# Kernel optimization log

Measured on AMD Instinct MI355X. Metric: run time of the kernel, lower is better.

## Reference

```python
import jax, jax.numpy as jnp
import numpy as np

D_MODEL = 1024
N_HEADS = 16
D_K = D_MODEL // N_HEADS
NEG = -1e10


def setup_inputs() -> dict:
    key = jax.random.key(0)
    ks = jax.random.split(key, 12)
    bs, sl = 2, 2048
    q = jax.random.normal(ks[0], (bs, sl, D_MODEL), dtype=jnp.float32)
    k = jax.random.normal(ks[1], (bs, sl, D_MODEL), dtype=jnp.float32)
    v = jax.random.normal(ks[2], (bs, sl, D_MODEL), dtype=jnp.float32)
    mask = jax.random.randint(ks[3], (bs, 1, sl, sl), 0, 2).astype(bool)
    s = 1.0 / np.sqrt(D_MODEL)
    Wq = jax.random.uniform(ks[4], (D_MODEL, D_MODEL), jnp.float32, -s, s)
    bq = jax.random.uniform(ks[5], (D_MODEL,), jnp.float32, -s, s)
    Wk = jax.random.uniform(ks[6], (D_MODEL, D_MODEL), jnp.float32, -s, s)
    bk = jax.random.uniform(ks[7], (D_MODEL,), jnp.float32, -s, s)
    Wv = jax.random.uniform(ks[8], (D_MODEL, D_MODEL), jnp.float32, -s, s)
    bv = jax.random.uniform(ks[9], (D_MODEL,), jnp.float32, -s, s)
    Wo = jax.random.uniform(ks[10], (D_MODEL, D_MODEL), jnp.float32, -s, s)
    bo = jax.random.uniform(ks[11], (D_MODEL,), jnp.float32, -s, s)
    return {"q": q, "k": k, "v": v, "mask": mask,
            "Wq": Wq, "bq": bq, "Wk": Wk, "bk": bk,
            "Wv": Wv, "bv": bv, "Wo": Wo, "bo": bo}


def reference(q, k, v, mask, Wq, bq, Wk, bk, Wv, bv, Wo, bo):
    bs, sl, _ = q.shape
    sl2 = k.shape[1]
    # linear projections (torch Linear: x @ W.T + b), split into heads: [b, h, s, d_k]
    qh = (q @ Wq.T + bq).reshape(bs, sl, N_HEADS, D_K).transpose(0, 2, 1, 3)
    kh = (k @ Wk.T + bk).reshape(bs, sl2, N_HEADS, D_K).transpose(0, 2, 1, 3)
    vh = (v @ Wv.T + bv).reshape(bs, sl2, N_HEADS, D_K).transpose(0, 2, 1, 3)
    scores = jnp.einsum('bhqd,bhkd->bhqk', qh, kh) / jnp.sqrt(jnp.float32(D_K))
    scores = jnp.where(mask, NEG, scores)
    attn = jax.nn.softmax(scores, axis=-1)
    z = jnp.einsum('bhqk,bhkd->bhqd', attn, vh)  # [b, h, sl, d_k]
    z = z.transpose(0, 2, 1, 3).reshape(bs, sl, D_MODEL)
    return z @ Wo.T + bo
```

## Files before the change

kernel.cpp:

```cpp
#include <hip/hip_runtime.h>

typedef __attribute__((ext_vector_type(8))) short short8;
typedef __attribute__((ext_vector_type(4))) float f32x4;
typedef __attribute__((ext_vector_type(16))) float f32x16;
typedef __attribute__((ext_vector_type(4))) unsigned int u32x4;

#define MFMA16(a, b, c) __builtin_amdgcn_mfma_f32_16x16x32_bf16((a), (b), (c), 0, 0, 0)
#define MFMA32(a, b, c) __builtin_amdgcn_mfma_f32_32x32x16_bf16((a), (b), (c), 0, 0, 0)

#if __has_builtin(__builtin_amdgcn_exp2f)
#define EXP2(x) __builtin_amdgcn_exp2f(x)
#else
#define EXP2(x) __expf((x) * 0.6931471805599453f)
#endif

__device__ __forceinline__ unsigned short f2bf(float f) {
  unsigned int u = __float_as_uint(f);
  u += 0x7FFFu + ((u >> 16) & 1u);
  return (unsigned short)(u >> 16);
}

__device__ __forceinline__ float bf2f(unsigned short u) {
  return __uint_as_float(((unsigned int)u) << 16);
}

__device__ __forceinline__ unsigned int cvtpk(float lo, float hi) {
  unsigned int r;
  asm("v_cvt_pk_bf16_f32 %0, %1, %2" : "=v"(r) : "v"(lo), "v"(hi));
  return r;
}

__device__ __forceinline__ short8 mk8(unsigned int a, unsigned int b,
                                      unsigned int c, unsigned int d) {
  u32x4 u = {a, b, c, d};
  return __builtin_bit_cast(short8, u);
}

__device__ __forceinline__ void gload16(const void* g, void* l) {
  __builtin_amdgcn_global_load_lds((const __attribute__((address_space(1))) void*)g,
                                   (__attribute__((address_space(3))) void*)l, 16, 0, 0);
}

__device__ __forceinline__ short8 fragld64(const unsigned short* base, int row, int kchunk) {
  int cc = kchunk ^ (row & 7);
  return *(const short8*)(base + row * 64 + cc * 8);
}

__global__ void cvt3(const float* __restrict__ a, const float* __restrict__ b,
                     const float* __restrict__ c, unsigned short* __restrict__ out, int n4) {
  const float* src = (blockIdx.z == 0) ? a : ((blockIdx.z == 1) ? b : c);
  int i = blockIdx.x * blockDim.x + threadIdx.x;
  if (i >= n4) return;
  float4 v = ((const float4*)src)[i];
  ushort4 o;
  o.x = f2bf(v.x); o.y = f2bf(v.y); o.z = f2bf(v.z); o.w = f2bf(v.w);
  ((ushort4*)(out + (size_t)blockIdx.z * (size_t)n4 * 4))[i] = o;
}

__global__ void cvt4(const float* __restrict__ a, const float* __restrict__ b,
                     const float* __restrict__ c, const float* __restrict__ d,
                     unsigned short* __restrict__ out, int n4) {
  const float* src = (blockIdx.z == 0) ? a : ((blockIdx.z == 1) ? b
                   : ((blockIdx.z == 2) ? c : d));
  int i = blockIdx.x * blockDim.x + threadIdx.x;
  if (i >= n4) return;
  float4 v = ((const float4*)src)[i];
  ushort4 o;
  o.x = f2bf(v.x); o.y = f2bf(v.y); o.z = f2bf(v.z); o.w = f2bf(v.w);
  ((ushort4*)(out + (size_t)blockIdx.z * (size_t)n4 * 4))[i] = o;
}

__global__ void maskpack(const int* __restrict__ m, unsigned long long* __restrict__ mw) {
  const int lane = threadIdx.x & 63;
  const size_t wbase = ((size_t)blockIdx.x * (blockDim.x >> 6) + (threadIdx.x >> 6)) * 4ull;
#pragma unroll
  for (int u = 0; u < 4; ++u) {
    size_t word = wbase + u;
    int x = m[word * 64 + lane];
    unsigned long long bb = __ballot(x != 0);
    if (lane == 0) mw[word] = bb;
  }
}

__global__ void vtrans(const unsigned short* __restrict__ vh, unsigned short* __restrict__ vtg) {
  __shared__ unsigned short t[64][66];
  const int sx = blockIdx.x * 64, h = blockIdx.y, b = blockIdx.z;
  const int tid = threadIdx.x;
  const int r = tid >> 2, c0 = (tid & 3) * 16;
  const unsigned short* src = vh + ((size_t)(b * 2048 + sx + r)) * 1024 + h * 64 + c0;
  short8 x0 = *(const short8*)src;
  short8 x1 = *(const short8*)(src + 8);
#pragma unroll
  for (int e = 0; e < 8; ++e) {
    t[c0 + e][r] = (unsigned short)x0[e];
    t[c0 + 8 + e][r] = (unsigned short)x1[e];
  }
  __syncthreads();
  short8 y0, y1;
#pragma unroll
  for (int e = 0; e < 8; ++e) {
    y0[e] = (short)t[r][c0 + e];
    y1[e] = (short)t[r][c0 + 8 + e];
  }
  unsigned short* dst = vtg + ((size_t)((b * 16 + h) * 64 + r)) * 2048 + sx + c0;
  *(short8*)dst = y0;
  *(short8*)(dst + 8) = y1;
}

template<bool OUT_BF16>
__global__ __launch_bounds__(256, 3) void gemm_bt(
    const unsigned short* __restrict__ Abase, const unsigned short* __restrict__ Bbase,
    const float* __restrict__ bias0, const float* __restrict__ bias1,
    const float* __restrict__ bias2, void* __restrict__ outv, float scale0)
{
  constexpr int K = 1024, N = 1024;
  const int z = blockIdx.z;
  const unsigned short* A = Abase + (size_t)z * 4194304ull;
  const unsigned short* B = Bbase + (size_t)z * 1048576ull;
  const float* bias = (z == 0) ? bias0 : ((z == 1) ? bias1 : bias2);
  const float scale = (z == 0) ? scale0 : 1.0f;

  __shared__ unsigned short ldsA[128 * 64];
  __shared__ unsigned short ldsB[128 * 64];

  const int tid = threadIdx.x;
  const int lane = tid & 63, wid = tid >> 6;
  const int c16 = lane & 15, g = lane >> 4;
  const int m0 = blockIdx.y * 128, n0 = blockIdx.x * 128;
  const int wr = (wid >> 1) * 64, wc = (wid & 1) * 64;

  f32x4 acc[4][4] = {};

  for (int kt = 0; kt < K; kt += 64) {
    __syncthreads();
#pragma unroll
    for (int i = 0; i < 4; ++i) {
      int row = i * 32 + (tid >> 3);
      int cc = tid & 7;
      int scc = cc ^ (row & 7);
      gload16(A + (size_t)(m0 + row) * K + kt + scc * 8, ldsA + row * 64 + cc * 8);
      gload16(B + (size_t)(n0 + row) * K + kt + scc * 8, ldsB + row * 64 + cc * 8);
    }
    __syncthreads();
#pragma unroll
    for (int kc = 0; kc < 2; ++kc) {
      short8 af[4], bf[4];
#pragma unroll
      for (int mi = 0; mi < 4; ++mi) af[mi] = fragld64(ldsA, wr + mi * 16 + c16, kc * 4 + g);
#pragma unroll
      for (int ni = 0; ni < 4; ++ni) bf[ni] = fragld64(ldsB, wc + ni * 16 + c16, kc * 4 + g);
#pragma unroll
      for (int mi = 0; mi < 4; ++mi)
#pragma unroll
        for (int ni = 0; ni < 4; ++ni)
          acc[mi][ni] = MFMA16(af[mi], bf[ni], acc[mi][ni]);
    }
  }

#pragma unroll
  for (int mi = 0; mi < 4; ++mi)
#pragma unroll
    for (int ni = 0; ni < 4; ++ni) {
      int col = n0 + wc + ni * 16 + c16;
      float bb = bias[col];
#pragma unroll
      for (int r = 0; r < 4; ++r) {
        int row = m0 + wr + mi * 16 + g * 4 + r;
        float v = (acc[mi][ni][r] + bb) * scale;
        if constexpr (OUT_BF16)
          ((unsigned short*)outv)[(size_t)z * 4194304ull + (size_t)row * N + col] = f2bf(v);
        else
          ((float*)outv)[(size_t)row * N + col] = v;
      }
    }
}

__device__ __forceinline__ void half_step(
    const unsigned short* __restrict__ kb, const unsigned short* __restrict__ vb,
    const short8 qf[4], unsigned int nb, int ql, int hd, int rowoff, int gm0,
    f32x16& z0, f32x16& z1, float& rs_out)
{
  f32x16 s;
#pragma unroll
  for (int m = 0; m < 4; ++m) {
    unsigned int nib = (nb >> (m * 8)) & 0xFu;
#pragma unroll
    for (int c = 0; c < 4; ++c)
      s[m * 4 + c] = ((nib >> c) & 1u) ? -1e10f : 0.0f;
  }
  __builtin_amdgcn_s_setprio(1);
#pragma unroll
  for (int kc = 0; kc < 4; ++kc)
    s = MFMA32(fragld64(kb, rowoff + ql, kc * 2 + hd), qf[kc], s);
  __builtin_amdgcn_s_setprio(0);
#pragma unroll
  for (int i = 0; i < 16; ++i) s[i] = EXP2(s[i]);
  {
    float a0 = (s[0] + s[1]) + (s[2] + s[3]);
    float a1 = (s[4] + s[5]) + (s[6] + s[7]);
    float a2 = (s[8] + s[9]) + (s[10] + s[11]);
    float a3 = (s[12] + s[13]) + (s[14] + s[15]);
    rs_out = (a0 + a1) + (a2 + a3);
  }
  unsigned int wv[8];
#pragma unroll
  for (int i = 0; i < 8; ++i) wv[i] = cvtpk(s[2 * i], s[2 * i + 1]);
  asm("v_permlane32_swap_b32 %0, %1" : "+v"(wv[0]), "+v"(wv[2]));
  asm("v_permlane32_swap_b32 %0, %1" : "+v"(wv[1]), "+v"(wv[3]));
  asm("v_permlane32_swap_b32 %0, %1" : "+v"(wv[4]), "+v"(wv[6]));
  asm("v_permlane32_swap_b32 %0, %1" : "+v"(wv[5]), "+v"(wv[7]));
  __builtin_amdgcn_s_setprio(1);
  {
    short8 pf0 = mk8(wv[0], wv[1], wv[2], wv[3]);
    z0 = MFMA32(pf0, fragld64(vb, ql, gm0 * 2 + hd), z0);
    z1 = MFMA32(pf0, fragld64(vb, 32 + ql, gm0 * 2 + hd), z1);
    short8 pf1 = mk8(wv[4], wv[5], wv[6], wv[7]);
    z0 = MFMA32(pf1, fragld64(vb, ql, (gm0 + 1) * 2 + hd), z0);
    z1 = MFMA32(pf1, fragld64(vb, 32 + ql, (gm0 + 1) * 2 + hd), z1);
  }
  __builtin_amdgcn_s_setprio(0);
}

__global__ __launch_bounds__(256, 3) void attn(
    const unsigned short* __restrict__ qh, const unsigned short* __restrict__ kh,
    const unsigned short* __restrict__ vtg, const unsigned long long* __restrict__ mw,
    unsigned short* __restrict__ zn, float* __restrict__ ml)
{
  constexpr int SL = 2048, DM = 1024;
  const int bid = blockIdx.x;
  const int g = bid & 31;
  const int u = bid >> 5;
  const int sp = u & 1;
  const int qt = u >> 1;
  const int h = g & 15, b = g >> 4;

  const int tid = threadIdx.x, lane = tid & 63, w = tid >> 6;
  const int ql = lane & 31, hd = lane >> 5;
  const int qa = qt * 128 + w * 32;

  __shared__ unsigned short kbuf[2][4096];
  __shared__ unsigned short vbuf[2][4096];

  short8 qf[4];
  {
    const size_t qrow = ((size_t)b * SL + qa + ql) * DM + (size_t)h * 64 + hd * 8;
#pragma unroll
    for (int kc = 0; kc < 4; ++kc)
      qf[kc] = *(const short8*)(qh + qrow + kc * 16);
  }

  f32x16 zacc0 = {}, zacc1 = {};
  float lrun = 0.f;

  const int t0 = sp * 16, t1e = t0 + 16;
  const unsigned long long* mwq = mw + ((size_t)b * SL + qa + ql) * (SL / 64);
  unsigned long long mwc = mwq[t0];

  const int kr = tid >> 3, cc = tid & 7;
  const int r0 = kr, r1 = kr + 32;
  const size_t kbase = (size_t)b * SL * DM + (size_t)h * 64;
  const size_t vbase = (size_t)((b * 16 + h) * 64) * (size_t)SL;
  const unsigned short* kp0 = kh + kbase + (size_t)(t0 * 64 + r0) * DM + (cc ^ (r0 & 7)) * 8;
  const unsigned short* kp1 = kh + kbase + (size_t)(t0 * 64 + r1) * DM + (cc ^ (r1 & 7)) * 8;
  const unsigned short* vp0 = vtg + vbase + (size_t)r0 * SL + t0 * 64 + (cc ^ (r0 & 7)) * 8;
  const unsigned short* vp1 = vtg + vbase + (size_t)r1 * SL + t0 * 64 + (cc ^ (r1 & 7)) * 8;

  gload16(kp0, kbuf[0] + r0 * 64 + cc * 8);
  gload16(kp1, kbuf[0] + r1 * 64 + cc * 8);
  gload16(vp0, vbuf[0] + r0 * 64 + cc * 8);
  gload16(vp1, vbuf[0] + r1 * 64 + cc * 8);

  for (int t = t0; t < t1e; ++t) {
    const int cur = t & 1, nxt = cur ^ 1;
    __syncthreads();

    const bool more = (t + 1 < t1e);
    unsigned long long mwn = 0;
    if (more) {
      kp0 += 64 * DM; kp1 += 64 * DM; vp0 += 64; vp1 += 64;
      gload16(kp0, kbuf[nxt] + r0 * 64 + cc * 8);
      gload16(kp1, kbuf[nxt] + r1 * 64 + cc * 8);
      gload16(vp0, vbuf[nxt] + r0 * 64 + cc * 8);
      gload16(vp1, vbuf[nxt] + r1 * 64 + cc * 8);
      mwn = mwq[t + 1];
    }

    float rsA, rsB;
    half_step(kbuf[cur], vbuf[cur], qf, ((unsigned int)mwc) >> (hd * 4),
              ql, hd, 0, 0, zacc0, zacc1, rsA);
    half_step(kbuf[cur], vbuf[cur], qf, ((unsigned int)(mwc >> 32)) >> (hd * 4),
              ql, hd, 32, 2, zacc0, zacc1, rsB);
    lrun += rsA + rsB;
    mwc = mwn;
  }

  lrun += __shfl_xor(lrun, 32);

  const int pbase = g * 2048 + qt * 128 + w * 32;
  float invl = (lrun > 0.f) ? 1.f / lrun : 0.f;
  if (hd == 0) ml[(size_t)(pbase + ql) * 2 + sp] = lrun;
#pragma unroll
  for (int reg = 0; reg < 16; ++reg) {
    int qrow = (reg & 3) + 8 * (reg >> 2) + 4 * hd;
    float il = __shfl(invl, qrow);
    size_t zr = ((size_t)(pbase + qrow) * 2 + sp) * 64;
    zn[zr + ql] = f2bf(zacc0[reg] * il);
    zn[zr + 32 + ql] = f2bf(zacc1[reg] * il);
  }
}

__global__ void combine(const unsigned short* __restrict__ zn, const float* __restrict__ ml,
                        unsigned short* __restrict__ zbf) {
  int idx = blockIdx.x * 256 + threadIdx.x;
  int p = idx >> 3, oct = idx & 7;
  float l1 = ml[(size_t)p * 2 + 0];
  float l2 = ml[(size_t)p * 2 + 1];
  float tot = l1 + l2;
  float inv = (tot > 0.f) ? 1.f / tot : 0.f;
  float w1 = l1 * inv, w2 = l2 * inv;
  short8 x1 = *(const short8*)(zn + ((size_t)p * 2 + 0) * 64 + oct * 8);
  short8 x2 = *(const short8*)(zn + ((size_t)p * 2 + 1) * 64 + oct * 8);
  int g = p >> 11, srow = p & 2047;
  int h = g & 15, b = g >> 4;
  unsigned short* dst = zbf + ((size_t)(b * 2048 + srow)) * 1024 + h * 64 + oct * 8;
  short8 o;
#pragma unroll
  for (int e = 0; e < 8; ++e)
    o[e] = (short)f2bf(w1 * bf2f((unsigned short)x1[e]) + w2 * bf2f((unsigned short)x2[e]));
  *(short8*)dst = o;
}

extern "C" void kernel_launch(void* const* d_in, const int* in_sizes, int n_in,
                              void* d_out, int out_size, void* d_ws, size_t ws_size,
                              hipStream_t stream) {
  const float* q  = (const float*)d_in[0];
  const float* k  = (const float*)d_in[1];
  const float* v  = (const float*)d_in[2];
  const int* mask = (const int*)d_in[3];
  const float* Wq = (const float*)d_in[4];
  const float* bq = (const float*)d_in[5];
  const float* Wk = (const float*)d_in[6];
  const float* bk = (const float*)d_in[7];
  const float* Wv = (const float*)d_in[8];
  const float* bv = (const float*)d_in[9];
  const float* Wo = (const float*)d_in[10];
  const float* bo = (const float*)d_in[11];

  char* ws = (char*)d_ws;
  unsigned short* xbf = (unsigned short*)ws;
  unsigned long long* mwb = (unsigned long long*)ws;
  unsigned short* zn  = (unsigned short*)(ws + 1048576);
  float* ml           = (float*)(ws + 17825792);
  unsigned short* wbf = (unsigned short*)(ws + 25165824);
  unsigned short* qkv = (unsigned short*)(ws + 33554432);
  unsigned short* vtg = (unsigned short*)(ws + 58720256);
  unsigned short* zbf = (unsigned short*)(ws + 58720256);

  cvt3<<<dim3(4096, 1, 3), 256, 0, stream>>>(q, k, v, xbf, 1048576);
  cvt4<<<dim3(1024, 1, 4), 256, 0, stream>>>(Wq, Wk, Wv, Wo, wbf, 262144);

  gemm_bt<true><<<dim3(8, 32, 3), 256, 0, stream>>>(xbf, wbf, bq, bk, bv, (void*)qkv,
                                                    0.125f * 1.44269504088896f);
  maskpack<<<8192, 256, 0, stream>>>(mask, mwb);
  vtrans<<<dim3(32, 16, 2), 256, 0, stream>>>(qkv + 8388608ull, vtg);
  attn<<<1024, 256, 0, stream>>>(qkv, qkv + 4194304ull, vtg, mwb, zn, ml);
  combine<<<2048, 256, 0, stream>>>(zn, ml, zbf);
  gemm_bt<false><<<dim3(8, 32, 1), 256, 0, stream>>>(zbf, wbf + 3145728ull, bo, bo, bo, d_out, 1.0f);
}
```

Before: 154.8 us.

## Drop split-KV attention and combine kernel; add XOR swizzle variant for LDS tiles

The attention kernel no longer splits the key sequence into two halves. Each block now walks all 32 key tiles and writes the normalized bf16 output straight into the head-interleaved buffer used by the output projection. This removes the separate combine kernel and the partial-output and row-sum traffic through global memory. The cost is half as many blocks (512 instead of 1024), so each CU has fewer waves to hide latency and each block runs a longer serial loop. Separately, the LDS swizzle now also XORs bits from row/8, which is meant to reduce bank conflicts in the GEMM and attention tile loads.

```diff
diff --git a/kernel.cpp b/kernel.cpp
--- a/kernel.cpp
+++ b/kernel.cpp
@@ -20,10 +20,6 @@
   return (unsigned short)(u >> 16);
 }
 
-__device__ __forceinline__ float bf2f(unsigned short u) {
-  return __uint_as_float(((unsigned int)u) << 16);
-}
-
 __device__ __forceinline__ unsigned int cvtpk(float lo, float hi) {
   unsigned int r;
   asm("v_cvt_pk_bf16_f32 %0, %1, %2" : "=v"(r) : "v"(lo), "v"(hi));
@@ -41,8 +37,12 @@
                                    (__attribute__((address_space(3))) void*)l, 16, 0, 0);
 }
 
+__device__ __forceinline__ int swz(int row) {
+  return (row & 7) ^ (((row >> 3) & 3) << 1);
+}
+
 __device__ __forceinline__ short8 fragld64(const unsigned short* base, int row, int kchunk) {
-  int cc = kchunk ^ (row & 7);
+  int cc = kchunk ^ swz(row);
   return *(const short8*)(base + row * 64 + cc * 8);
 }
 
@@ -137,7 +137,7 @@
     for (int i = 0; i < 4; ++i) {
       int row = i * 32 + (tid >> 3);
       int cc = tid & 7;
-      int scc = cc ^ (row & 7);
+      int scc = cc ^ swz(row);
       gload16(A + (size_t)(m0 + row) * K + kt + scc * 8, ldsA + row * 64 + cc * 8);
       gload16(B + (size_t)(n0 + row) * K + kt + scc * 8, ldsB + row * 64 + cc * 8);
     }
@@ -224,14 +224,12 @@
 __global__ __launch_bounds__(256, 3) void attn(
     const unsigned short* __restrict__ qh, const unsigned short* __restrict__ kh,
     const unsigned short* __restrict__ vtg, const unsigned long long* __restrict__ mw,
-    unsigned short* __restrict__ zn, float* __restrict__ ml)
+    unsigned short* __restrict__ zbf)
 {
-  constexpr int SL = 2048, DM = 1024;
+  constexpr int SL = 2048, DM = 1024, NT = SL / 64;
   const int bid = blockIdx.x;
   const int g = bid & 31;
-  const int u = bid >> 5;
-  const int sp = u & 1;
-  const int qt = u >> 1;
+  const int qt = bid >> 5;
   const int h = g & 15, b = g >> 4;
 
   const int tid = threadIdx.x, lane = tid & 63, w = tid >> 6;
@@ -252,29 +250,28 @@
   f32x16 zacc0 = {}, zacc1 = {};
   float lrun = 0.f;
 
-  const int t0 = sp * 16, t1e = t0 + 16;
   const unsigned long long* mwq = mw + ((size_t)b * SL + qa + ql) * (SL / 64);
-  unsigned long long mwc = mwq[t0];
+  unsigned long long mwc = mwq[0];
 
   const int kr = tid >> 3, cc = tid & 7;
   const int r0 = kr, r1 = kr + 32;
   const size_t kbase = (size_t)b * SL * DM + (size_t)h * 64;
   const size_t vbase = (size_t)((b * 16 + h) * 64) * (size_t)SL;
-  const unsigned short* kp0 = kh + kbase + (size_t)(t0 * 64 + r0) * DM + (cc ^ (r0 & 7)) * 8;
-  const unsigned short* kp1 = kh + kbase + (size_t)(t0 * 64 + r1) * DM + (cc ^ (r1 & 7)) * 8;
-  const unsigned short* vp0 = vtg + vbase + (size_t)r0 * SL + t0 * 64 + (cc ^ (r0 & 7)) * 8;
-  const unsigned short* vp1 = vtg + vbase + (size_t)r1 * SL + t0 * 64 + (cc ^ (r1 & 7)) * 8;
+  const unsigned short* kp0 = kh + kbase + (size_t)r0 * DM + (cc ^ swz(r0)) * 8;
+  const unsigned short* kp1 = kh + kbase + (size_t)r1 * DM + (cc ^ swz(r1)) * 8;
+  const unsigned short* vp0 = vtg + vbase + (size_t)r0 * SL + (cc ^ swz(r0)) * 8;
+  const unsigned short* vp1 = vtg + vbase + (size_t)r1 * SL + (cc ^ swz(r1)) * 8;
 
   gload16(kp0, kbuf[0] + r0 * 64 + cc * 8);
   gload16(kp1, kbuf[0] + r1 * 64 + cc * 8);
   gload16(vp0, vbuf[0] + r0 * 64 + cc * 8);
   gload16(vp1, vbuf[0] + r1 * 64 + cc * 8);
 
-  for (int t = t0; t < t1e; ++t) {
+  for (int t = 0; t < NT; ++t) {
     const int cur = t & 1, nxt = cur ^ 1;
     __syncthreads();
 
-    const bool more = (t + 1 < t1e);
+    const bool more = (t + 1 < NT);
     unsigned long long mwn = 0;
     if (more) {
       kp0 += 64 * DM; kp1 += 64 * DM; vp0 += 64; vp1 += 64;
@@ -296,38 +293,15 @@
 
   lrun += __shfl_xor(lrun, 32);
 
-  const int pbase = g * 2048 + qt * 128 + w * 32;
   float invl = (lrun > 0.f) ? 1.f / lrun : 0.f;
-  if (hd == 0) ml[(size_t)(pbase + ql) * 2 + sp] = lrun;
 #pragma unroll
   for (int reg = 0; reg < 16; ++reg) {
     int qrow = (reg & 3) + 8 * (reg >> 2) + 4 * hd;
     float il = __shfl(invl, qrow);
-    size_t zr = ((size_t)(pbase + qrow) * 2 + sp) * 64;
-    zn[zr + ql] = f2bf(zacc0[reg] * il);
-    zn[zr + 32 + ql] = f2bf(zacc1[reg] * il);
-  }
-}
-
-__global__ void combine(const unsigned short* __restrict__ zn, const float* __restrict__ ml,
-                        unsigned short* __restrict__ zbf) {
-  int idx = blockIdx.x * 256 + threadIdx.x;
-  int p = idx >> 3, oct = idx & 7;
-  float l1 = ml[(size_t)p * 2 + 0];
-  float l2 = ml[(size_t)p * 2 + 1];
-  float tot = l1 + l2;
-  float inv = (tot > 0.f) ? 1.f / tot : 0.f;
-  float w1 = l1 * inv, w2 = l2 * inv;
-  short8 x1 = *(const short8*)(zn + ((size_t)p * 2 + 0) * 64 + oct * 8);
-  short8 x2 = *(const short8*)(zn + ((size_t)p * 2 + 1) * 64 + oct * 8);
-  int g = p >> 11, srow = p & 2047;
-  int h = g & 15, b = g >> 4;
-  unsigned short* dst = zbf + ((size_t)(b * 2048 + srow)) * 1024 + h * 64 + oct * 8;
-  short8 o;
-#pragma unroll
-  for (int e = 0; e < 8; ++e)
-    o[e] = (short)f2bf(w1 * bf2f((unsigned short)x1[e]) + w2 * bf2f((unsigned short)x2[e]));
-  *(short8*)dst = o;
+    size_t orow = ((size_t)b * SL + qa + qrow) * DM + (size_t)h * 64;
+    zbf[orow + ql] = f2bf(zacc0[reg] * il);
+    zbf[orow + 32 + ql] = f2bf(zacc1[reg] * il);
+  }
 }
 
 extern "C" void kernel_launch(void* const* d_in, const int* in_sizes, int n_in,
@@ -349,12 +323,10 @@
   char* ws = (char*)d_ws;
   unsigned short* xbf = (unsigned short*)ws;
   unsigned long long* mwb = (unsigned long long*)ws;
-  unsigned short* zn  = (unsigned short*)(ws + 1048576);
-  float* ml           = (float*)(ws + 17825792);
+  unsigned short* zbf = (unsigned short*)(ws + 2097152);
   unsigned short* wbf = (unsigned short*)(ws + 25165824);
   unsigned short* qkv = (unsigned short*)(ws + 33554432);
   unsigned short* vtg = (unsigned short*)(ws + 58720256);
-  unsigned short* zbf = (unsigned short*)(ws + 58720256);
 
   cvt3<<<dim3(4096, 1, 3), 256, 0, stream>>>(q, k, v, xbf, 1048576);
   cvt4<<<dim3(1024, 1, 4), 256, 0, stream>>>(Wq, Wk, Wv, Wo, wbf, 262144);
@@ -363,7 +335,6 @@
                                                     0.125f * 1.44269504088896f);
   maskpack<<<8192, 256, 0, stream>>>(mask, mwb);
   vtrans<<<dim3(32, 16, 2), 256, 0, stream>>>(qkv + 8388608ull, vtg);
-  attn<<<1024, 256, 0, stream>>>(qkv, qkv + 4194304ull, vtg, mwb, zn, ml);
-  combine<<<2048, 256, 0, stream>>>(zn, ml, zbf);
+  attn<<<512, 256, 0, stream>>>(qkv, qkv + 4194304ull, vtg, mwb, zbf);
   gemm_bt<false><<<dim3(8, 32, 1), 256, 0, stream>>>(zbf, wbf + 3145728ull, bo, bo, bo, d_out, 1.0f);
 }
```

Result: faster. 148.0 us (-4.4%).
